# Optimization experiments

Hardware: AMD Instinct MI355X
Metric: run time of the kernel (lower is better)

The kernel has to match this reference:

```python
import jax, jax.numpy as jnp
import numpy as np

N_NODES = 200000
N_EDGES = 500000
F_IN = 165
HIDDEN = 384
OUT = 2


def setup_inputs() -> dict:
    key = jax.random.key(0)
    ks = jax.random.split(key, 8)
    x = jax.random.normal(ks[0], (N_NODES, F_IN), dtype=jnp.float32)
    edge_index = jax.random.randint(ks[1], (2, N_EDGES), 0, N_NODES, dtype=jnp.int64)
    # Glorot-ish init for GCNConv weights, zero bias (PyG default)
    def glorot(k, fan_in, fan_out):
        lim = (6.0 / (fan_in + fan_out)) ** 0.5
        return jax.random.uniform(k, (fan_in, fan_out), dtype=jnp.float32, minval=-lim, maxval=lim)
    W1 = glorot(ks[2], F_IN, HIDDEN)
    b1 = jnp.zeros((HIDDEN,), dtype=jnp.float32)
    W2 = glorot(ks[3], HIDDEN, HIDDEN)
    b2 = jnp.zeros((HIDDEN,), dtype=jnp.float32)
    W3 = glorot(ks[4], HIDDEN, OUT)
    b3 = jnp.zeros((OUT,), dtype=jnp.float32)
    return {"x": x, "edge_index": edge_index,
            "W1": W1, "b1": b1, "W2": W2, "b2": b2, "W3": W3, "b3": b3}


def _gcn_norm(edge_index, num_nodes):
    # PyG gcn_norm: add self-loops, symmetric normalization D^-1/2 (A+I) D^-1/2
    loop = jnp.arange(num_nodes, dtype=edge_index.dtype)
    row = jnp.concatenate([edge_index[0], loop])
    col = jnp.concatenate([edge_index[1], loop])
    ones = jnp.ones(row.shape[0], dtype=jnp.float32)
    deg = jax.ops.segment_sum(ones, col, num_segments=num_nodes)
    dinv = jnp.where(deg > 0, jax.lax.rsqrt(deg), 0.0)
    norm = dinv[row] * dinv[col]  # [E + N]
    return row, col, norm


def _gcn_conv(h, W, b, row, col, norm, num_nodes):
    h = h @ W                          # [N, F_out] linear transform first
    msg = h[row] * norm[:, None]       # gather + scale, [E+N, F_out]
    agg = jax.ops.segment_sum(msg, col, num_segments=num_nodes)
    return agg + b


def reference(x, edge_index, W1, b1, W2, b2, W3, b3):
    n = x.shape[0]
    row, col, norm = _gcn_norm(edge_index, n)
    h = jax.nn.relu(_gcn_conv(x, W1, b1, row, col, norm, n))
    h = jax.nn.relu(_gcn_conv(h, W2, b2, row, col, norm, n))
    return _gcn_conv(h, W3, b3, row, col, norm, n)
```

## Files before the change

kernel.cpp:

```cpp
#include <hip/hip_runtime.h>
#include <hip/hip_bf16.h>

#define N_NODES 200000
#define N_EDGES 500000
#define F_IN    165
#define HIDDEN  384
#define F_OUT   2

#define KPAD1   192
#define M_TILES 1563
#define M_PAD   (M_TILES * 128)
#define NB_SCAN 782
#define GRID_GEMM (196 * 24)

typedef unsigned short ushort_t;
typedef unsigned int   uint_t;

using bf16x8 = __attribute__((ext_vector_type(8))) short;
using f32x4  = __attribute__((ext_vector_type(4))) float;

__device__ __forceinline__ float bf2f(uint_t u) {
    return __uint_as_float(u << 16);
}
__device__ __forceinline__ ushort_t f2bf(float x) {
    uint_t b = __float_as_uint(x);
    return (ushort_t)((b + 0x7FFFu + ((b >> 16) & 1u)) >> 16);
}

__device__ __forceinline__ void async16(const ushort_t* g, ushort_t* l) {
    __builtin_amdgcn_global_load_lds(
        (const __attribute__((address_space(1))) void*)g,
        (__attribute__((address_space(3))) void*)l,
        16, 0, 0);
}

__global__ void count_kernel(const int* __restrict__ col, int* __restrict__ cnt, int E) {
    int e = blockIdx.x * blockDim.x + threadIdx.x;
    if (e < E) atomicAdd(&cnt[col[e]], 1);
}

__global__ void dinv_kernel(const int* __restrict__ cnt, float* __restrict__ dinv, int n) {
    int i = blockIdx.x * blockDim.x + threadIdx.x;
    if (i < n) dinv[i] = rsqrtf((float)(cnt[i] + 1));
}

__global__ __launch_bounds__(256) void scan1_kernel(const int* __restrict__ cnt,
                                                    int* __restrict__ loc,
                                                    int* __restrict__ bsum, int N) {
    __shared__ int sh[256];
    int t = threadIdx.x;
    int i = blockIdx.x * 256 + t;
    int v = (i < N) ? cnt[i] : 0;
    sh[t] = v;
    __syncthreads();
    #pragma unroll
    for (int off = 1; off < 256; off <<= 1) {
        int u = (t >= off) ? sh[t - off] : 0;
        __syncthreads();
        sh[t] += u;
        __syncthreads();
    }
    int incl = sh[t];
    if (i < N) loc[i] = incl - v;
    if (t == 255) bsum[blockIdx.x] = incl;
}

__global__ __launch_bounds__(1024) void scan2_kernel(int* __restrict__ bsum, int NB) {
    __shared__ int sh[1024];
    int t = threadIdx.x;
    int v = (t < NB) ? bsum[t] : 0;
    sh[t] = v;
    __syncthreads();
    #pragma unroll
    for (int off = 1; off < 1024; off <<= 1) {
        int u = (t >= off) ? sh[t - off] : 0;
        __syncthreads();
        sh[t] += u;
        __syncthreads();
    }
    if (t < NB) bsum[t] = sh[t] - v;
}

__global__ __launch_bounds__(256) void scan3_kernel(int* __restrict__ ptr,
                                                    int* __restrict__ cursor,
                                                    const int* __restrict__ bsum,
                                                    int N, int E) {
    int t = threadIdx.x;
    int i = blockIdx.x * 256 + t;
    if (i < N) {
        int p = ptr[i] + bsum[blockIdx.x];
        ptr[i] = p;
        cursor[i] = p;
    }
    if (i == 0) ptr[N] = E;
}

__global__ void scatter_kernel(const int* __restrict__ row, const int* __restrict__ col,
                               const float* __restrict__ dinv,
                               int* __restrict__ cursor,
                               int* __restrict__ row_srt, float* __restrict__ nrm_srt, int E) {
    int e = blockIdx.x * blockDim.x + threadIdx.x;
    if (e >= E) return;
    int r = row[e], c = col[e];
    int pos = atomicAdd(&cursor[c], 1);
    row_srt[pos] = r;
    nrm_srt[pos] = dinv[r] * dinv[c];
}

__global__ void convx_kernel(const float* __restrict__ X, uint_t* __restrict__ Xb, int total) {
    int idx = blockIdx.x * blockDim.x + threadIdx.x;
    if (idx >= total) return;
    int node = idx / 96, ui = idx - node * 96;
    int f = ui * 2;
    const float* xr = X + (size_t)node * F_IN;
    float lo = (f < F_IN) ? xr[f] : 0.0f;
    float hi = (f + 1 < F_IN) ? xr[f + 1] : 0.0f;
    Xb[idx] = (uint_t)f2bf(lo) | ((uint_t)f2bf(hi) << 16);
}

__global__ __launch_bounds__(256) void agg165b_kernel(
        const uint_t* __restrict__ Xb, const float* __restrict__ dinv,
        const int* __restrict__ ptr, const int* __restrict__ row_srt,
        const float* __restrict__ nrm_srt, ushort_t* __restrict__ out, int N) {
    int w    = (blockIdx.x * blockDim.x + threadIdx.x) >> 6;
    int lane = threadIdx.x & 63;
    if (w >= N) return;
    float d2 = dinv[w]; d2 *= d2;
    const uint_t* self = Xb + (size_t)w * 96;
    bool two = (lane < 19);
    uint_t u0 = self[lane];
    uint_t u1 = two ? self[64 + lane] : 0u;
    float ax0 = bf2f(u0 & 0xFFFFu) * d2, ay0 = bf2f(u0 >> 16) * d2;
    float ax1 = bf2f(u1 & 0xFFFFu) * d2, ay1 = bf2f(u1 >> 16) * d2;
    int e0 = ptr[w], e1 = ptr[w + 1];
    for (int e = e0; e < e1; ++e) {
        int r = row_srt[e];
        float wg = nrm_srt[e];
        const uint_t* hr = Xb + (size_t)r * 96;
        uint_t v0 = hr[lane];
        uint_t v1 = two ? hr[64 + lane] : 0u;
        ax0 = fmaf(bf2f(v0 & 0xFFFFu), wg, ax0);
        ay0 = fmaf(bf2f(v0 >> 16), wg, ay0);
        ax1 = fmaf(bf2f(v1 & 0xFFFFu), wg, ax1);
        ay1 = fmaf(bf2f(v1 >> 16), wg, ay1);
    }
    uint_t* o = (uint_t*)(out + (size_t)w * KPAD1);
    o[lane] = (uint_t)f2bf(ax0) | ((uint_t)f2bf(ay0) << 16);
    if (two) o[64 + lane] = (uint_t)f2bf(ax1) | ((uint_t)f2bf(ay1) << 16);
}

__global__ __launch_bounds__(256) void agg384_kernel(
        const ushort_t* __restrict__ H, const float* __restrict__ dinv,
        const int* __restrict__ ptr, const int* __restrict__ row_srt,
        const float* __restrict__ nrm_srt, ushort_t* __restrict__ out, int N) {
    int w    = (blockIdx.x * blockDim.x + threadIdx.x) >> 6;
    int lane = threadIdx.x & 63;
    if (w >= N) return;
    float d2 = dinv[w]; d2 *= d2;
    const uint_t* self = (const uint_t*)(H + (size_t)w * HIDDEN);
    float ax[3], ay[3];
    #pragma unroll
    for (int j = 0; j < 3; ++j) {
        uint_t u = self[lane + 64 * j];
        ax[j] = bf2f(u & 0xFFFFu) * d2;
        ay[j] = bf2f(u >> 16) * d2;
    }
    int e0 = ptr[w], e1 = ptr[w + 1];
    for (int e = e0; e < e1; ++e) {
        int r = row_srt[e];
        float wg = nrm_srt[e];
        const uint_t* hr = (const uint_t*)(H + (size_t)r * HIDDEN);
        #pragma unroll
        for (int j = 0; j < 3; ++j) {
            uint_t u = hr[lane + 64 * j];
            ax[j] = fmaf(bf2f(u & 0xFFFFu), wg, ax[j]);
            ay[j] = fmaf(bf2f(u >> 16), wg, ay[j]);
        }
    }
    uint_t* o = (uint_t*)(out + (size_t)w * HIDDEN);
    #pragma unroll
    for (int j = 0; j < 3; ++j)
        o[lane + 64 * j] = (uint_t)f2bf(ax[j]) | ((uint_t)f2bf(ay[j]) << 16);
}

__global__ void prep_wt_kernel(const float* __restrict__ W, ushort_t* __restrict__ Wt,
                               int Kin, int Kpad, int Nn) {
    int idx = blockIdx.x * blockDim.x + threadIdx.x;
    if (idx >= Nn * Kpad) return;
    int n = idx / Kpad, k = idx - n * Kpad;
    float v = (k < Kin) ? W[(size_t)k * Nn + n] : 0.0f;
    Wt[idx] = f2bf(v);
}

#define GBK 32

template<bool RELU>
__global__ __launch_bounds__(256) void mfma_gemm_kernel(
        const ushort_t* __restrict__ A, const ushort_t* __restrict__ Wt,
        const float* __restrict__ bias, ushort_t* __restrict__ C,
        int Ks, int Nn, int nTilesM) {
    __shared__ ushort_t As[3][128 * GBK];
    __shared__ ushort_t Bs[3][128 * GBK];

    const int l  = blockIdx.x;
    const int g  = l / 24;
    const int r_ = l - g * 24;
    const int cb = r_ >> 3;
    const int pm = r_ & 7;
    const int pt = g * 8 + pm;
    if (pt >= nTilesM) return;
    const int bm = pt * 128;
    const int bn = cb * 128;

    const int tid  = threadIdx.x;
    const int lane = tid & 63;
    const int w    = tid >> 6;
    const int wm   = w & 1;
    const int wn   = w >> 1;

    auto brow = [](int s) {
        return ((s >> 6) * 64) + ((s & 63) >> 4) + ((s & 15) * 4);
    };

    const int r0  = w * 32;
    const int s0  = r0 + (lane >> 2);
    const int s1  = s0 + 16;
    const int c0  = (lane & 3) ^ ((s0 >> 1) & 3);
    const int c1  = (lane & 3) ^ ((s1 >> 1) & 3);

    const ushort_t* gA0 = A + (size_t)(bm + s0) * Ks + c0 * 8;
    const ushort_t* gA1 = A + (size_t)(bm + s1) * Ks + c1 * 8;
    const ushort_t* gB0 = Wt + (size_t)(bn + brow(s0)) * Ks + c0 * 8;
    const ushort_t* gB1 = Wt + (size_t)(bn + brow(s1)) * Ks + c1 * 8;

    const int p     = lane & 15;
    const int khalf = lane >> 4;
    const int qf    = khalf ^ ((p >> 1) & 3);
    int aoff[4], boff[4];
    #pragma unroll
    for (int f = 0; f < 4; ++f) {
        aoff[f] = (wm * 64 + f * 16 + p) * GBK + qf * 8;
        boff[f] = (wn * 64 + f * 16 + p) * GBK + qf * 8;
    }

    f32x4 acc[4][4] = {};

    const int ksteps = Ks >> 5;
    #pragma unroll
    for (int t = 0; t < 3; ++t) {
        if (t < ksteps) {
            const int ko = t * GBK;
            async16(gA0 + ko, &As[t][r0 * GBK]);
            async16(gA1 + ko, &As[t][(r0 + 16) * GBK]);
            async16(gB0 + ko, &Bs[t][r0 * GBK]);
            async16(gB1 + ko, &Bs[t][(r0 + 16) * GBK]);
        }
    }

    int cur = 0;
    for (int kt = 0; kt < ksteps; ++kt) {
        const int ahead = ((ksteps - kt) < 3 ? (ksteps - kt) : 3) - 1;
        if (ahead == 2)      asm volatile("s_waitcnt vmcnt(8)" ::: "memory");
        else if (ahead == 1) asm volatile("s_waitcnt vmcnt(4)" ::: "memory");
        else                 asm volatile("s_waitcnt vmcnt(0)" ::: "memory");
        asm volatile("s_barrier" ::: "memory");

        const ushort_t* Ab = As[cur];
        const ushort_t* Bb = Bs[cur];
        bf16x8 af[4], bfr[4];
        #pragma unroll
        for (int f = 0; f < 4; ++f) {
            af[f]  = *reinterpret_cast<const bf16x8*>(&Ab[aoff[f]]);
            bfr[f] = *reinterpret_cast<const bf16x8*>(&Bb[boff[f]]);
        }
        #pragma unroll
        for (int mi = 0; mi < 4; ++mi)
            #pragma unroll
            for (int ni = 0; ni < 4; ++ni)
                acc[mi][ni] = __builtin_amdgcn_mfma_f32_16x16x32_bf16(
                    af[mi], bfr[ni], acc[mi][ni], 0, 0, 0);

        asm volatile("s_barrier" ::: "memory");
        if (kt + 3 < ksteps) {
            const int ko = (kt + 3) * GBK;
            async16(gA0 + ko, &As[cur][r0 * GBK]);
            async16(gA1 + ko, &As[cur][(r0 + 16) * GBK]);
            async16(gB0 + ko, &Bs[cur][r0 * GBK]);
            async16(gB1 + ko, &Bs[cur][(r0 + 16) * GBK]);
        }
        cur = (cur == 2) ? 0 : cur + 1;
    }

    const int colbase = bn + wn * 64 + p * 4;
    const float4 bb = *reinterpret_cast<const float4*>(bias + colbase);
    const float bias4[4] = {bb.x, bb.y, bb.z, bb.w};
    #pragma unroll
    for (int mi = 0; mi < 4; ++mi) {
        const int rowbase = bm + wm * 64 + mi * 16 + khalf * 4;
        #pragma unroll
        for (int j = 0; j < 4; ++j) {
            float v0 = acc[mi][0][j] + bias4[0];
            float v1 = acc[mi][1][j] + bias4[1];
            float v2 = acc[mi][2][j] + bias4[2];
            float v3 = acc[mi][3][j] + bias4[3];
            if (RELU) {
                v0 = fmaxf(v0, 0.f); v1 = fmaxf(v1, 0.f);
                v2 = fmaxf(v2, 0.f); v3 = fmaxf(v3, 0.f);
            }
            ushort4 o;
            o.x = f2bf(v0); o.y = f2bf(v1); o.z = f2bf(v2); o.w = f2bf(v3);
            *reinterpret_cast<ushort4*>(C + (size_t)(rowbase + j) * Nn + colbase) = o;
        }
    }
}

__global__ __launch_bounds__(256) void gemm_n2_kernel(
        const ushort_t* __restrict__ A, const float* __restrict__ W,
        float* __restrict__ G, int M) {
    int w    = (blockIdx.x * blockDim.x + threadIdx.x) >> 6;
    int lane = threadIdx.x & 63;
    if (w >= M) return;
    const uint_t* a = (const uint_t*)(A + (size_t)w * HIDDEN);
    float s0 = 0.f, s1 = 0.f;
    #pragma unroll
    for (int j = 0; j < 3; ++j) {
        int f2 = lane + 64 * j;
        uint_t u = a[f2];
        float alo = bf2f(u & 0xFFFFu), ahi = bf2f(u >> 16);
        int k = f2 * 2;
        s0 = fmaf(alo, W[k * 2 + 0], s0);
        s1 = fmaf(alo, W[k * 2 + 1], s1);
        s0 = fmaf(ahi, W[k * 2 + 2], s0);
        s1 = fmaf(ahi, W[k * 2 + 3], s1);
    }
    #pragma unroll
    for (int off = 32; off; off >>= 1) {
        s0 += __shfl_down(s0, off);
        s1 += __shfl_down(s1, off);
    }
    if (lane == 0) { G[(size_t)w * 2] = s0; G[(size_t)w * 2 + 1] = s1; }
}

__global__ void out_kernel(const float* __restrict__ G, const float* __restrict__ dinv,
                           const int* __restrict__ ptr, const int* __restrict__ row_srt,
                           const float* __restrict__ nrm_srt, const float* __restrict__ b3,
                           float* __restrict__ out, int N) {
    int i = blockIdx.x * blockDim.x + threadIdx.x;
    if (i >= N) return;
    float d2 = dinv[i]; d2 *= d2;
    float a0 = G[(size_t)i * 2 + 0] * d2 + b3[0];
    float a1 = G[(size_t)i * 2 + 1] * d2 + b3[1];
    int e0 = ptr[i], e1 = ptr[i + 1];
    for (int e = e0; e < e1; ++e) {
        int r = row_srt[e];
        float wg = nrm_srt[e];
        a0 = fmaf(G[(size_t)r * 2 + 0], wg, a0);
        a1 = fmaf(G[(size_t)r * 2 + 1], wg, a1);
    }
    out[(size_t)i * 2 + 0] = a0;
    out[(size_t)i * 2 + 1] = a1;
}

extern "C" void kernel_launch(void* const* d_in, const int* in_sizes, int n_in,
                              void* d_out, int out_size, void* d_ws, size_t ws_size,
                              hipStream_t stream) {
    const float* x   = (const float*)d_in[0];
    const int*   ei  = (const int*)  d_in[1];
    const float* W1  = (const float*)d_in[2];
    const float* b1  = (const float*)d_in[3];
    const float* W2  = (const float*)d_in[4];
    const float* b2  = (const float*)d_in[5];
    const float* W3  = (const float*)d_in[6];
    const float* b3  = (const float*)d_in[7];
    float* out = (float*)d_out;

    const int N = N_NODES, E = N_EDGES;
    const int* row = ei;
    const int* col = ei + E;

    size_t off = 0;
    auto alloc = [&](size_t bytes) { size_t o = off; off += (bytes + 255) & ~(size_t)255; return o; };
    size_t o_dinv   = alloc((size_t)N * 4);
    size_t o_ptr    = alloc((size_t)(N + 1) * 4);
    size_t o_cnt    = alloc((size_t)N * 4);
    size_t o_cursor = alloc((size_t)N * 4);
    size_t o_bsum   = alloc((size_t)NB_SCAN * 4);
    size_t o_rowsrt = alloc((size_t)E * 4);
    size_t o_nrmsrt = alloc((size_t)E * 4);
    size_t o_G      = alloc((size_t)N * 2 * 4);
    size_t o_Wt1    = alloc((size_t)HIDDEN * KPAD1 * 2);
    size_t o_Wt2    = alloc((size_t)HIDDEN * HIDDEN * 2);
    size_t o_B1     = alloc((size_t)M_PAD * HIDDEN * 2);
    size_t o_B2     = alloc((size_t)M_PAD * HIDDEN * 2);
    if (ws_size < off) return;

    char* ws = (char*)d_ws;
    float*    dinv    = (float*)(ws + o_dinv);
    int*      ptr     = (int*)  (ws + o_ptr);
    int*      cnt     = (int*)  (ws + o_cnt);
    int*      cursor  = (int*)  (ws + o_cursor);
    int*      bsum    = (int*)  (ws + o_bsum);
    int*      row_srt = (int*)  (ws + o_rowsrt);
    float*    nrm_srt = (float*)(ws + o_nrmsrt);
    float*    G       = (float*)(ws + o_G);
    ushort_t* Wt1     = (ushort_t*)(ws + o_Wt1);
    ushort_t* Wt2     = (ushort_t*)(ws + o_Wt2);
    ushort_t* B1      = (ushort_t*)(ws + o_B1);
    ushort_t* B2      = (ushort_t*)(ws + o_B2);
    uint_t*   Xb      = (uint_t*)B2;

    const int B = 256;

    prep_wt_kernel<<<(HIDDEN * KPAD1 + B - 1) / B, B, 0, stream>>>(W1, Wt1, F_IN, KPAD1, HIDDEN);
    prep_wt_kernel<<<(HIDDEN * HIDDEN + B - 1) / B, B, 0, stream>>>(W2, Wt2, HIDDEN, HIDDEN, HIDDEN);
    convx_kernel<<<(N * 96 + B - 1) / B, B, 0, stream>>>(x, Xb, N * 96);

    hipMemsetAsync(cnt, 0, (size_t)N * 4, stream);
    count_kernel<<<(E + B - 1) / B, B, 0, stream>>>(col, cnt, E);
    dinv_kernel<<<(N + B - 1) / B, B, 0, stream>>>(cnt, dinv, N);
    scan1_kernel<<<NB_SCAN, 256, 0, stream>>>(cnt, ptr, bsum, N);
    scan2_kernel<<<1, 1024, 0, stream>>>(bsum, NB_SCAN);
    scan3_kernel<<<NB_SCAN, 256, 0, stream>>>(ptr, cursor, bsum, N, E);
    scatter_kernel<<<(E + B - 1) / B, B, 0, stream>>>(row, col, dinv, cursor, row_srt, nrm_srt, E);

    agg165b_kernel<<<(N * 64 + B - 1) / B, B, 0, stream>>>(Xb, dinv, ptr, row_srt, nrm_srt, B1, N);

    mfma_gemm_kernel<true><<<GRID_GEMM, 256, 0, stream>>>(B1, Wt1, b1, B2, KPAD1, HIDDEN, M_TILES);

    agg384_kernel<<<(N * 64 + B - 1) / B, B, 0, stream>>>(B2, dinv, ptr, row_srt, nrm_srt, B1, N);

    mfma_gemm_kernel<true><<<GRID_GEMM, 256, 0, stream>>>(B1, Wt2, b2, B2, HIDDEN, HIDDEN, M_TILES);

    gemm_n2_kernel<<<(N * 64 + B - 1) / B, B, 0, stream>>>(B2, W3, G, N);

    out_kernel<<<(N + B - 1) / B, B, 0, stream>>>(G, dinv, ptr, row_srt, nrm_srt, b3, out, N);
}
```

Baseline: 507.7 us.

## Fuse layer-3 linear projection into layer-2 GEMM epilogue with atomics

Replaces the second MFMA GEMM plus the separate N=2 projection kernel with one GEMM whose epilogue applies bias and ReLU, projects onto W3, reduces across lanes and atomically adds the partial results into G. This skips writing and re-reading the 200000x384 bf16 hidden activation and drops one launch. In exchange G must be zeroed with an extra memset, each row takes three atomic contributions (one per column block), and summation order becomes nondeterministic.

```diff
diff --git a/kernel.cpp b/kernel.cpp
--- a/kernel.cpp
+++ b/kernel.cpp
@@ -314,31 +314,135 @@
     }
 }
 
-__global__ __launch_bounds__(256) void gemm_n2_kernel(
-        const ushort_t* __restrict__ A, const float* __restrict__ W,
-        float* __restrict__ G, int M) {
-    int w    = (blockIdx.x * blockDim.x + threadIdx.x) >> 6;
-    int lane = threadIdx.x & 63;
-    if (w >= M) return;
-    const uint_t* a = (const uint_t*)(A + (size_t)w * HIDDEN);
-    float s0 = 0.f, s1 = 0.f;
-    #pragma unroll
-    for (int j = 0; j < 3; ++j) {
-        int f2 = lane + 64 * j;
-        uint_t u = a[f2];
-        float alo = bf2f(u & 0xFFFFu), ahi = bf2f(u >> 16);
-        int k = f2 * 2;
-        s0 = fmaf(alo, W[k * 2 + 0], s0);
-        s1 = fmaf(alo, W[k * 2 + 1], s1);
-        s0 = fmaf(ahi, W[k * 2 + 2], s0);
-        s1 = fmaf(ahi, W[k * 2 + 3], s1);
-    }
-    #pragma unroll
-    for (int off = 32; off; off >>= 1) {
-        s0 += __shfl_down(s0, off);
-        s1 += __shfl_down(s1, off);
-    }
-    if (lane == 0) { G[(size_t)w * 2] = s0; G[(size_t)w * 2 + 1] = s1; }
+__global__ __launch_bounds__(256) void mfma_gemm_fused_kernel(
+        const ushort_t* __restrict__ A, const ushort_t* __restrict__ Wt,
+        const float* __restrict__ bias, const float* __restrict__ W3,
+        float* __restrict__ G, int Ks, int Nn, int nTilesM) {
+    __shared__ ushort_t As[3][128 * GBK];
+    __shared__ ushort_t Bs[3][128 * GBK];
+
+    const int l  = blockIdx.x;
+    const int g  = l / 24;
+    const int r_ = l - g * 24;
+    const int cb = r_ >> 3;
+    const int pm = r_ & 7;
+    const int pt = g * 8 + pm;
+    if (pt >= nTilesM) return;
+    const int bm = pt * 128;
+    const int bn = cb * 128;
+
+    const int tid  = threadIdx.x;
+    const int lane = tid & 63;
+    const int w    = tid >> 6;
+    const int wm   = w & 1;
+    const int wn   = w >> 1;
+
+    auto brow = [](int s) {
+        return ((s >> 6) * 64) + ((s & 63) >> 4) + ((s & 15) * 4);
+    };
+
+    const int r0  = w * 32;
+    const int s0  = r0 + (lane >> 2);
+    const int s1  = s0 + 16;
+    const int c0  = (lane & 3) ^ ((s0 >> 1) & 3);
+    const int c1  = (lane & 3) ^ ((s1 >> 1) & 3);
+
+    const ushort_t* gA0 = A + (size_t)(bm + s0) * Ks + c0 * 8;
+    const ushort_t* gA1 = A + (size_t)(bm + s1) * Ks + c1 * 8;
+    const ushort_t* gB0 = Wt + (size_t)(bn + brow(s0)) * Ks + c0 * 8;
+    const ushort_t* gB1 = Wt + (size_t)(bn + brow(s1)) * Ks + c1 * 8;
+
+    const int p     = lane & 15;
+    const int khalf = lane >> 4;
+    const int qf    = khalf ^ ((p >> 1) & 3);
+    int aoff[4], boff[4];
+    #pragma unroll
+    for (int f = 0; f < 4; ++f) {
+        aoff[f] = (wm * 64 + f * 16 + p) * GBK + qf * 8;
+        boff[f] = (wn * 64 + f * 16 + p) * GBK + qf * 8;
+    }
+
+    f32x4 acc[4][4] = {};
+
+    const int ksteps = Ks >> 5;
+    #pragma unroll
+    for (int t = 0; t < 3; ++t) {
+        if (t < ksteps) {
+            const int ko = t * GBK;
+            async16(gA0 + ko, &As[t][r0 * GBK]);
+            async16(gA1 + ko, &As[t][(r0 + 16) * GBK]);
+            async16(gB0 + ko, &Bs[t][r0 * GBK]);
+            async16(gB1 + ko, &Bs[t][(r0 + 16) * GBK]);
+        }
+    }
+
+    int cur = 0;
+    for (int kt = 0; kt < ksteps; ++kt) {
+        const int ahead = ((ksteps - kt) < 3 ? (ksteps - kt) : 3) - 1;
+        if (ahead == 2)      asm volatile("s_waitcnt vmcnt(8)" ::: "memory");
+        else if (ahead == 1) asm volatile("s_waitcnt vmcnt(4)" ::: "memory");
+        else                 asm volatile("s_waitcnt vmcnt(0)" ::: "memory");
+        asm volatile("s_barrier" ::: "memory");
+
+        const ushort_t* Ab = As[cur];
+        const ushort_t* Bb = Bs[cur];
+        bf16x8 af[4], bfr[4];
+        #pragma unroll
+        for (int f = 0; f < 4; ++f) {
+            af[f]  = *reinterpret_cast<const bf16x8*>(&Ab[aoff[f]]);
+            bfr[f] = *reinterpret_cast<const bf16x8*>(&Bb[boff[f]]);
+        }
+        #pragma unroll
+        for (int mi = 0; mi < 4; ++mi)
+            #pragma unroll
+            for (int ni = 0; ni < 4; ++ni)
+                acc[mi][ni] = __builtin_amdgcn_mfma_f32_16x16x32_bf16(
+                    af[mi], bfr[ni], acc[mi][ni], 0, 0, 0);
+
+        asm volatile("s_barrier" ::: "memory");
+        if (kt + 3 < ksteps) {
+            const int ko = (kt + 3) * GBK;
+            async16(gA0 + ko, &As[cur][r0 * GBK]);
+            async16(gA1 + ko, &As[cur][(r0 + 16) * GBK]);
+            async16(gB0 + ko, &Bs[cur][r0 * GBK]);
+            async16(gB1 + ko, &Bs[cur][(r0 + 16) * GBK]);
+        }
+        cur = (cur == 2) ? 0 : cur + 1;
+    }
+
+    const int colbase = bn + wn * 64 + p * 4;
+    const float4 bb = *reinterpret_cast<const float4*>(bias + colbase);
+    const float bias4[4] = {bb.x, bb.y, bb.z, bb.w};
+    float w30[4], w31[4];
+    #pragma unroll
+    for (int ni = 0; ni < 4; ++ni) {
+        w30[ni] = W3[(size_t)(colbase + ni) * 2 + 0];
+        w31[ni] = W3[(size_t)(colbase + ni) * 2 + 1];
+    }
+    #pragma unroll
+    for (int mi = 0; mi < 4; ++mi) {
+        const int rowbase = bm + wm * 64 + mi * 16 + khalf * 4;
+        #pragma unroll
+        for (int j = 0; j < 4; ++j) {
+            float g0 = 0.f, g1 = 0.f;
+            #pragma unroll
+            for (int ni = 0; ni < 4; ++ni) {
+                float h = fmaxf(acc[mi][ni][j] + bias4[ni], 0.f);
+                g0 = fmaf(h, w30[ni], g0);
+                g1 = fmaf(h, w31[ni], g1);
+            }
+            #pragma unroll
+            for (int m = 1; m < 16; m <<= 1) {
+                g0 += __shfl_xor(g0, m);
+                g1 += __shfl_xor(g1, m);
+            }
+            const int r = rowbase + j;
+            if (p == 0 && r < N_NODES) {
+                atomicAdd(&G[(size_t)r * 2 + 0], g0);
+                atomicAdd(&G[(size_t)r * 2 + 1], g1);
+            }
+        }
+    }
 }
 
 __global__ void out_kernel(const float* __restrict__ G, const float* __restrict__ dinv,
@@ -416,6 +520,7 @@
     convx_kernel<<<(N * 96 + B - 1) / B, B, 0, stream>>>(x, Xb, N * 96);
 
     hipMemsetAsync(cnt, 0, (size_t)N * 4, stream);
+    hipMemsetAsync(G, 0, (size_t)N * 2 * 4, stream);
     count_kernel<<<(E + B - 1) / B, B, 0, stream>>>(col, cnt, E);
     dinv_kernel<<<(N + B - 1) / B, B, 0, stream>>>(cnt, dinv, N);
     scan1_kernel<<<NB_SCAN, 256, 0, stream>>>(cnt, ptr, bsum, N);
@@ -429,9 +534,7 @@
 
     agg384_kernel<<<(N * 64 + B - 1) / B, B, 0, stream>>>(B2, dinv, ptr, row_srt, nrm_srt, B1, N);
 
-    mfma_gemm_kernel<true><<<GRID_GEMM, 256, 0, stream>>>(B1, Wt2, b2, B2, HIDDEN, HIDDEN, M_TILES);
-
-    gemm_n2_kernel<<<(N * 64 + B - 1) / B, B, 0, stream>>>(B2, W3, G, N);
+    mfma_gemm_fused_kernel<<<GRID_GEMM, 256, 0, stream>>>(B1, Wt2, b2, W3, G, HIDDEN, HIDDEN, M_TILES);
 
     out_kernel<<<(N + B - 1) / B, B, 0, stream>>>(G, dinv, ptr, row_srt, nrm_srt, b3, out, N);
 }
```

Result: faster. 497.0 us, median of 2 (-2.1%).
